# Performance work log

Measured on AMD Instinct MI355X. Metric: run time of the kernel, lower is better.

## Reference

```python
import jax, jax.numpy as jnp
import numpy as np


def setup_inputs() -> dict:
    key = jax.random.key(0)
    k1, k2, k3, k4 = jax.random.split(key, 4)
    H = W = D = 192
    I = jax.random.normal(k1, (1, 1, H, W, D), dtype=jnp.float32)
    dx_t = jax.random.normal(k2, (1, H, W, D), dtype=jnp.float32)
    dy_t = jax.random.normal(k3, (1, H, W, D), dtype=jnp.float32)
    dz_t = jax.random.normal(k4, (1, H, W, D), dtype=jnp.float32)
    return {"I": I, "dx_t": dx_t, "dy_t": dy_t, "dz_t": dz_t}


def reference(I, dx_t, dy_t, dz_t):
    # Trilinear warp, faithful to the torch module (valid for batch=1).
    B, C, H, W, D = I.shape
    # Identity meshgrid: x varies along width (axis 1), y along height (axis 0),
    # z along depth (axis 2) -- matches the numpy construction in __init__.
    x_mesh = jnp.arange(W, dtype=jnp.float32)[None, :, None]
    y_mesh = jnp.arange(H, dtype=jnp.float32)[:, None, None]
    z_mesh = jnp.arange(D, dtype=jnp.float32)[None, None, :]
    # +1 accounts for the zero-padding of I by 1 voxel on every side.
    x = dx_t[0] + x_mesh + 1.0  # [H,W,D]
    y = dy_t[0] + y_mesh + 1.0
    z = dz_t[0] + z_mesh + 1.0

    Ip = jnp.pad(I[0], ((0, 0), (1, 1), (1, 1), (1, 1)))  # [C,H+2,W+2,D+2]
    Hp, Wp, Dp = H + 2, W + 2, D + 2

    fx = jnp.floor(x).astype(jnp.int32)
    fy = jnp.floor(y).astype(jnp.int32)
    fz = jnp.floor(z).astype(jnp.int32)
    x0 = jnp.clip(fx, 0, Wp - 1); x1 = jnp.clip(fx + 1, 0, Wp - 1)
    y0 = jnp.clip(fy, 0, Hp - 1); y1 = jnp.clip(fy + 1, 0, Hp - 1)
    z0 = jnp.clip(fz, 0, Dp - 1); z1 = jnp.clip(fz + 1, 0, Dp - 1)

    # Fractional weights computed from the *clamped* upper corner (faithful).
    dx = x1.astype(jnp.float32) - x
    dy = y1.astype(jnp.float32) - y
    dz = z1.astype(jnp.float32) - z

    # Gather 8 corners: padded volume layout is [C, y, x, z].
    Ia = Ip[:, y0, x0, z0]
    Ib = Ip[:, y1, x0, z0]
    Ic = Ip[:, y0, x1, z0]
    Id = Ip[:, y1, x1, z0]
    Ie = Ip[:, y0, x0, z1]
    If = Ip[:, y1, x0, z1]
    Ig = Ip[:, y0, x1, z1]
    Ih = Ip[:, y1, x1, z1]

    wa = dz * dx * dy
    wb = dz * dx * (1 - dy)
    wc = dz * (1 - dx) * dy
    wd = dz * (1 - dx) * (1 - dy)
    we = (1 - dz) * dx * dy
    wf = (1 - dz) * dx * (1 - dy)
    wg = (1 - dz) * (1 - dx) * dy
    wh = (1 - dz) * (1 - dx) * (1 - dy)

    out = (wa * Ia + wb * Ib + wc * Ic + wd * Id
           + we * Ie + wf * If + wg * Ig + wh * Ih)  # [C,H,W,D]
    return out[None]  # [1,C,H,W,D]
```

## Files before the change

### kernel.cpp

```cpp
#include <hip/hip_runtime.h>

constexpr int H = 192, W = 192, D = 192;
constexpr int BH = 16, BW = 16, BZ = 16;
constexpr int TY = 24, TX = 24, TZ = 28;
constexpr int TILE_N = TY * TX * TZ;
constexpr int NINSTR = TY * TX * (TZ / 4) / 64;

__device__ __forceinline__ float ref_voxel(const float* __restrict__ I,
                                           float x, float y, float zf)
{
    int fx = (int)floorf(x), fy = (int)floorf(y), fz = (int)floorf(zf);
    int x0 = min(max(fx, 0), W + 1), x1 = min(max(fx + 1, 0), W + 1);
    int y0 = min(max(fy, 0), H + 1), y1 = min(max(fy + 1, 0), H + 1);
    int zp0 = min(max(fz, 0), D + 1), zp1 = min(max(fz + 1, 0), D + 1);
    float dx = (float)x1 - x, dy = (float)y1 - y, dz = (float)zp1 - zf;
    int xi0 = x0 - 1, xi1 = x1 - 1, yi0 = y0 - 1, yi1 = y1 - 1;
    int zi = zp0 - 1, zj = zp1 - 1;
    float ax0 = ((unsigned)xi0 < (unsigned)W) ? dx       : 0.f;
    float ax1 = ((unsigned)xi1 < (unsigned)W) ? 1.f - dx : 0.f;
    float ay0 = ((unsigned)yi0 < (unsigned)H) ? dy       : 0.f;
    float ay1 = ((unsigned)yi1 < (unsigned)H) ? 1.f - dy : 0.f;
    float az0 = ((unsigned)zi  < (unsigned)D) ? dz       : 0.f;
    float az1 = ((unsigned)zj  < (unsigned)D) ? 1.f - dz : 0.f;
    int xc0 = min(max(xi0, 0), W - 1), xc1 = min(max(xi1, 0), W - 1);
    int yc0 = min(max(yi0, 0), H - 1), yc1 = min(max(yi1, 0), H - 1);
    int zc0 = min(max(zi, 0), D - 1),  zc1 = min(max(zj, 0), D - 1);
    const float* r00 = I + (yc0 * W + xc0) * D;
    const float* r01 = I + (yc0 * W + xc1) * D;
    const float* r10 = I + (yc1 * W + xc0) * D;
    const float* r11 = I + (yc1 * W + xc1) * D;
    float s00 = az0 * r00[zc0] + az1 * r00[zc1];
    float s01 = az0 * r01[zc0] + az1 * r01[zc1];
    float s10 = az0 * r10[zc0] + az1 * r10[zc1];
    float s11 = az0 * r11[zc0] + az1 * r11[zc1];
    return ay0 * (ax0 * s00 + ax1 * s01) + ay1 * (ax0 * s10 + ax1 * s11);
}

__global__ __launch_bounds__(512) void st_tile(
    const float* __restrict__ I,
    const float* __restrict__ dxt,
    const float* __restrict__ dyt,
    const float* __restrict__ dzt,
    float* __restrict__ out)
{
    __shared__ float tile[TILE_N];

    const int tid = threadIdx.x;
    const int bx = blockIdx.x, by = blockIdx.y, bz = blockIdx.z;
    const int w0 = bx * BW, h0 = by * BH, z0 = bz * BZ;
    const int xg0 = w0 - 4, yg0 = h0 - 4, zg0 = z0 - 4;

    {
        const unsigned wv = tid >> 6, lane = tid & 63;
        for (unsigned i = wv; i < (unsigned)NINSTR; i += 8) {
            unsigned c = i * 64u + lane;
            unsigned row = c / 7u;
            unsigned s = c - row * 7u;
            unsigned ry = row / 24u;
            unsigned rx = row - ry * 24u;
            int gy = min(max(yg0 + (int)ry, 0), H - 1);
            int gx = min(max(xg0 + (int)rx, 0), W - 1);
            int zs = min(max(zg0 + (int)(s * 4u), 0), D - 4);
            const float* src = I + ((gy * W + gx) * D + zs);
            __builtin_amdgcn_global_load_lds(
                (const __attribute__((address_space(1))) void*)src,
                (__attribute__((address_space(3))) void*)(tile + i * 256u),
                16, 0, 0);
        }
    }

    const int zq = tid & 3, wloc = (tid >> 2) & 15, hl0 = tid >> 6;
    const int wg = w0 + wloc;
    float4 vx[2], vy[2], vz[2];
    #pragma unroll
    for (int k = 0; k < 2; ++k) {
        int hg = h0 + hl0 + 8 * k;
        int t4 = (hg * W + wg) * (D / 4) + (z0 >> 2) + zq;
        vx[k] = reinterpret_cast<const float4*>(dxt)[t4];
        vy[k] = reinterpret_cast<const float4*>(dyt)[t4];
        vz[k] = reinterpret_cast<const float4*>(dzt)[t4];
    }

    asm volatile("s_waitcnt vmcnt(0)" ::: "memory");
    __syncthreads();

    const int lox = max(0, -xg0), hix = min(TX - 2, 190 - xg0);
    const int loy = max(0, -yg0), hiy = min(TY - 2, 190 - yg0);
    const int loz = max(0, -zg0), hiz = min(TZ - 2, 190 - zg0);

    float ro[2][4];
    #pragma unroll
    for (int k = 0; k < 2; ++k) {
        const int hg = h0 + hl0 + 8 * k;
        const int hl = hl0 + 8 * k;
        float rxj[4] = {vx[k].x, vx[k].y, vx[k].z, vx[k].w};
        float ryj[4] = {vy[k].x, vy[k].y, vy[k].z, vy[k].w};
        float rzj[4] = {vz[k].x, vz[k].y, vz[k].z, vz[k].w};

        int   lxa[4], lya[4], lza[4];
        float txa[4], tya[4], tza[4];
        bool  fa[4];
        #pragma unroll
        for (int j = 0; j < 4; ++j) {
            float xl = rxj[j] + (float)(wloc + 4);
            float yl = ryj[j] + (float)(hl + 4);
            float zl = rzj[j] + (float)(zq * 4 + j + 4);
            float fxf = floorf(xl), fyf = floorf(yl), fzf = floorf(zl);
            lxa[j] = (int)fxf; lya[j] = (int)fyf; lza[j] = (int)fzf;
            txa[j] = xl - fxf; tya[j] = yl - fyf; tza[j] = zl - fzf;
            fa[j] = ((unsigned)(lxa[j] - lox) <= (unsigned)(hix - lox))
                  & ((unsigned)(lya[j] - loy) <= (unsigned)(hiy - loy))
                  & ((unsigned)(lza[j] - loz) <= (unsigned)(hiz - loz));
        }

        if (__builtin_expect(__all(fa[0] & fa[1] & fa[2] & fa[3]), 1)) {
            #pragma unroll
            for (int j = 0; j < 4; ++j) {
                int b = (lya[j] * TX + lxa[j]) * TZ + lza[j];
                float a0 = tile[b],                a1 = tile[b + 1];
                float b0 = tile[b + TZ],           b1 = tile[b + TZ + 1];
                float c0 = tile[b + TX * TZ],      c1 = tile[b + TX * TZ + 1];
                float d0 = tile[b + TX * TZ + TZ], d1 = tile[b + TX * TZ + TZ + 1];
                float wz0 = 1.f - tza[j], wz1 = tza[j];
                float wx0 = 1.f - txa[j], wx1 = txa[j];
                float wy0 = 1.f - tya[j], wy1 = tya[j];
                float s00 = wz0 * a0 + wz1 * a1;
                float s01 = wz0 * b0 + wz1 * b1;
                float s10 = wz0 * c0 + wz1 * c1;
                float s11 = wz0 * d0 + wz1 * d1;
                ro[k][j] = wy0 * (wx0 * s00 + wx1 * s01) + wy1 * (wx0 * s10 + wx1 * s11);
            }
        } else {
            #pragma unroll
            for (int j = 0; j < 4; ++j) {
                const int zv = z0 + zq * 4 + j;
                float x  = rxj[j] + (float)(wg + 1);
                float y  = ryj[j] + (float)(hg + 1);
                float zf = rzj[j] + (float)(zv + 1);

                int fx = (int)floorf(x), fy = (int)floorf(y), fz = (int)floorf(zf);
                int x0 = min(max(fx, 0), W + 1), x1 = min(max(fx + 1, 0), W + 1);
                int y0 = min(max(fy, 0), H + 1), y1 = min(max(fy + 1, 0), H + 1);
                int zp0 = min(max(fz, 0), D + 1), zp1 = min(max(fz + 1, 0), D + 1);

                float dx = (float)x1 - x, dy = (float)y1 - y, dz = (float)zp1 - zf;

                int xi0 = x0 - 1, xi1 = x1 - 1, yi0 = y0 - 1, yi1 = y1 - 1;
                int zi = zp0 - 1, zj2 = zp1 - 1;

                float ax0 = ((unsigned)xi0 < (unsigned)W) ? dx       : 0.f;
                float ax1 = ((unsigned)xi1 < (unsigned)W) ? 1.f - dx : 0.f;
                float ay0 = ((unsigned)yi0 < (unsigned)H) ? dy       : 0.f;
                float ay1 = ((unsigned)yi1 < (unsigned)H) ? 1.f - dy : 0.f;
                float az0 = ((unsigned)zi  < (unsigned)D) ? dz       : 0.f;
                float az1 = ((unsigned)zj2 < (unsigned)D) ? 1.f - dz : 0.f;

                int xc0 = min(max(xi0, 0), W - 1), xc1 = min(max(xi1, 0), W - 1);
                int yc0 = min(max(yi0, 0), H - 1), yc1 = min(max(yi1, 0), H - 1);
                int zc  = min(max(zi, 0), D - 2);

                bool zlo = (zi <= D - 2);
                bool zhi = (zi >= 0);

                int lx0 = xc0 - xg0, lx1 = xc1 - xg0;
                int ly0 = yc0 - yg0, ly1 = yc1 - yg0;
                int lz  = zc - zg0;

                bool ok = ((unsigned)lx0 <= (unsigned)(TX - 1))
                        & ((unsigned)lx1 <= (unsigned)(TX - 1))
                        & ((unsigned)ly0 <= (unsigned)(TY - 1))
                        & ((unsigned)ly1 <= (unsigned)(TY - 1))
                        & ((unsigned)lz  <= (unsigned)(TZ - 2));

                int b00 = min(max((ly0 * TX + lx0) * TZ + lz, 0), TILE_N - 2);
                int b01 = min(max((ly0 * TX + lx1) * TZ + lz, 0), TILE_N - 2);
                int b10 = min(max((ly1 * TX + lx0) * TZ + lz, 0), TILE_N - 2);
                int b11 = min(max((ly1 * TX + lx1) * TZ + lz, 0), TILE_N - 2);

                float a0 = tile[b00], a1 = tile[b00 + 1];
                float b0 = tile[b01], b1 = tile[b01 + 1];
                float c0 = tile[b10], c1 = tile[b10 + 1];
                float d0 = tile[b11], d1 = tile[b11 + 1];

                float v000 = zlo ? a0 : a1, v001 = zhi ? a1 : a0;
                float v010 = zlo ? b0 : b1, v011 = zhi ? b1 : b0;
                float v100 = zlo ? c0 : c1, v101 = zhi ? c1 : c0;
                float v110 = zlo ? d0 : d1, v111 = zhi ? d1 : d0;
                float s00 = az0 * v000 + az1 * v001;
                float s01 = az0 * v010 + az1 * v011;
                float s10 = az0 * v100 + az1 * v101;
                float s11 = az0 * v110 + az1 * v111;
                float r = ay0 * (ax0 * s00 + ax1 * s01)
                        + ay1 * (ax0 * s10 + ax1 * s11);

                ro[k][j] = __builtin_expect(ok, 1) ? r : ref_voxel(I, x, y, zf);
            }
        }
    }

    #pragma unroll
    for (int k = 0; k < 2; ++k) {
        int hg = h0 + hl0 + 8 * k;
        int t4 = (hg * W + wg) * (D / 4) + (z0 >> 2) + zq;
        reinterpret_cast<float4*>(out)[t4] =
            make_float4(ro[k][0], ro[k][1], ro[k][2], ro[k][3]);
    }
}

extern "C" void kernel_launch(void* const* d_in, const int* in_sizes, int n_in,
                              void* d_out, int out_size, void* d_ws, size_t ws_size,
                              hipStream_t stream) {
    const float* I   = (const float*)d_in[0];
    const float* dxt = (const float*)d_in[1];
    const float* dyt = (const float*)d_in[2];
    const float* dzt = (const float*)d_in[3];
    float* out = (float*)d_out;

    dim3 grid(W / BW, H / BH, D / BZ);
    hipLaunchKernelGGL(st_tile, grid, dim3(512), 0, stream,
                       I, dxt, dyt, dzt, out);
}
```

Measured before the change: 50.00 us.

## Shrink LDS halo tile and split staging to overlap second half with compute

Shrinks the staged halo tile from 24x24x28 to 23x23x24, with an asymmetric x/y halo, to cut LDS usage and global loads per block. Staging is split into two phases: the first 40 load instructions plus the first half's displacement loads are waited on with a partial vmcnt, and the first half computes while the remaining tile rows arrive. Launch bounds now request 6 blocks per CU for more occupancy. The smaller halo pushes more voxels onto the slow fallback path, and the hand-counted vmcnt values are fragile.

Result: slower. 102.5 us (+104.9%).

```diff
diff --git a/kernel.cpp b/kernel.cpp
--- a/kernel.cpp
+++ b/kernel.cpp
@@ -2,9 +2,11 @@
 
 constexpr int H = 192, W = 192, D = 192;
 constexpr int BH = 16, BW = 16, BZ = 16;
-constexpr int TY = 24, TX = 24, TZ = 28;
-constexpr int TILE_N = TY * TX * TZ;
-constexpr int NINSTR = TY * TX * (TZ / 4) / 64;
+constexpr int TY = 23, TX = 23, TZ = 24;
+constexpr int TILE_DATA = TY * TX * TZ;
+constexpr int LDS_DWORDS = 3264 * 4;
+constexpr int BMAX = TILE_DATA - 2;
+constexpr int NB1 = 40;
 
 __device__ __forceinline__ float ref_voxel(const float* __restrict__ I,
                                            float x, float y, float zf)
@@ -36,74 +38,91 @@
     return ay0 * (ax0 * s00 + ax1 * s01) + ay1 * (ax0 * s10 + ax1 * s11);
 }
 
-__global__ __launch_bounds__(512) void st_tile(
+__device__ __forceinline__ void stage_instr(const float* __restrict__ I, float* tile,
+                                            unsigned i, unsigned lane,
+                                            int xg0, int yg0, int zg0)
+{
+    unsigned c = i * 64u + lane;
+    unsigned row = c / 6u;
+    unsigned s = c - row * 6u;
+    unsigned ry = row / 23u;
+    unsigned rx = row - ry * 23u;
+    int gy = min(max(yg0 + (int)min(ry, 22u), 0), H - 1);
+    int gx = min(max(xg0 + (int)rx, 0), W - 1);
+    int zs = min(max(zg0 + (int)(s * 4u), 0), D - 4);
+    const float* src = I + ((gy * W + gx) * D + zs);
+    __builtin_amdgcn_global_load_lds(
+        (const __attribute__((address_space(1))) void*)src,
+        (__attribute__((address_space(3))) void*)(tile + i * 256u),
+        16, 0, 0);
+}
+
+__global__ __launch_bounds__(512, 6) void st_tile(
     const float* __restrict__ I,
     const float* __restrict__ dxt,
     const float* __restrict__ dyt,
     const float* __restrict__ dzt,
     float* __restrict__ out)
 {
-    __shared__ float tile[TILE_N];
+    __shared__ float tile[LDS_DWORDS];
 
     const int tid = threadIdx.x;
     const int bx = blockIdx.x, by = blockIdx.y, bz = blockIdx.z;
     const int w0 = bx * BW, h0 = by * BH, z0 = bz * BZ;
-    const int xg0 = w0 - 4, yg0 = h0 - 4, zg0 = z0 - 4;
-
-    {
-        const unsigned wv = tid >> 6, lane = tid & 63;
-        for (unsigned i = wv; i < (unsigned)NINSTR; i += 8) {
-            unsigned c = i * 64u + lane;
-            unsigned row = c / 7u;
-            unsigned s = c - row * 7u;
-            unsigned ry = row / 24u;
-            unsigned rx = row - ry * 24u;
-            int gy = min(max(yg0 + (int)ry, 0), H - 1);
-            int gx = min(max(xg0 + (int)rx, 0), W - 1);
-            int zs = min(max(zg0 + (int)(s * 4u), 0), D - 4);
-            const float* src = I + ((gy * W + gx) * D + zs);
-            __builtin_amdgcn_global_load_lds(
-                (const __attribute__((address_space(1))) void*)src,
-                (__attribute__((address_space(3))) void*)(tile + i * 256u),
-                16, 0, 0);
-        }
-    }
-
+    const int xg0 = w0 - 3, yg0 = h0 - 3, zg0 = z0 - 4;
+
+    const unsigned wv = tid >> 6, lane = tid & 63;
     const int zq = tid & 3, wloc = (tid >> 2) & 15, hl0 = tid >> 6;
     const int wg = w0 + wloc;
-    float4 vx[2], vy[2], vz[2];
+
     #pragma unroll
-    for (int k = 0; k < 2; ++k) {
-        int hg = h0 + hl0 + 8 * k;
-        int t4 = (hg * W + wg) * (D / 4) + (z0 >> 2) + zq;
-        vx[k] = reinterpret_cast<const float4*>(dxt)[t4];
-        vy[k] = reinterpret_cast<const float4*>(dyt)[t4];
-        vz[k] = reinterpret_cast<const float4*>(dzt)[t4];
-    }
-
-    asm volatile("s_waitcnt vmcnt(0)" ::: "memory");
-    __syncthreads();
+    for (unsigned t = 0; t < 5; ++t)
+        stage_instr(I, tile, wv + 8u * t, lane, xg0, yg0, zg0);
+    __builtin_amdgcn_sched_barrier(0);
+
+    const int t40 = ((h0 + hl0) * W + wg) * (D / 4) + (z0 >> 2) + zq;
+    float4 vx0 = reinterpret_cast<const float4*>(dxt)[t40];
+    float4 vy0 = reinterpret_cast<const float4*>(dyt)[t40];
+    float4 vz0 = reinterpret_cast<const float4*>(dzt)[t40];
+    __builtin_amdgcn_sched_barrier(0);
+
+    stage_instr(I, tile, 40u + wv, lane, xg0, yg0, zg0);
+    if (wv < 3) stage_instr(I, tile, 48u + wv, lane, xg0, yg0, zg0);
+    __builtin_amdgcn_sched_barrier(0);
+
+    const int t41 = ((h0 + 8 + hl0) * W + wg) * (D / 4) + (z0 >> 2) + zq;
+    float4 vx1 = reinterpret_cast<const float4*>(dxt)[t41];
+    float4 vy1 = reinterpret_cast<const float4*>(dyt)[t41];
+    float4 vz1 = reinterpret_cast<const float4*>(dzt)[t41];
+    __builtin_amdgcn_sched_barrier(0);
+
+    asm volatile("s_waitcnt vmcnt(4)" ::: "memory");
+    __builtin_amdgcn_s_barrier();
+    __builtin_amdgcn_sched_barrier(0);
 
     const int lox = max(0, -xg0), hix = min(TX - 2, 190 - xg0);
     const int loy = max(0, -yg0), hiy = min(TY - 2, 190 - yg0);
     const int loz = max(0, -zg0), hiz = min(TZ - 2, 190 - zg0);
 
-    float ro[2][4];
     #pragma unroll
-    for (int k = 0; k < 2; ++k) {
-        const int hg = h0 + hl0 + 8 * k;
-        const int hl = hl0 + 8 * k;
-        float rxj[4] = {vx[k].x, vx[k].y, vx[k].z, vx[k].w};
-        float ryj[4] = {vy[k].x, vy[k].y, vy[k].z, vy[k].w};
-        float rzj[4] = {vz[k].x, vz[k].y, vz[k].z, vz[k].w};
+    for (int half = 0; half < 2; ++half) {
+        const int hl = hl0 + half * 8;
+        const int hg = h0 + hl;
+        float4 vx = half ? vx1 : vx0;
+        float4 vy = half ? vy1 : vy0;
+        float4 vz = half ? vz1 : vz0;
+        float rxj[4] = {vx.x, vx.y, vx.z, vx.w};
+        float ryj[4] = {vy.x, vy.y, vy.z, vy.w};
+        float rzj[4] = {vz.x, vz.y, vz.z, vz.w};
+        float ro[4];
 
         int   lxa[4], lya[4], lza[4];
         float txa[4], tya[4], tza[4];
         bool  fa[4];
         #pragma unroll
         for (int j = 0; j < 4; ++j) {
-            float xl = rxj[j] + (float)(wloc + 4);
-            float yl = ryj[j] + (float)(hl + 4);
+            float xl = rxj[j] + (float)(wloc + 3);
+            float yl = ryj[j] + (float)(hl + 3);
             float zl = rzj[j] + (float)(zq * 4 + j + 4);
             float fxf = floorf(xl), fyf = floorf(yl), fzf = floorf(zl);
             lxa[j] = (int)fxf; lya[j] = (int)fyf; lza[j] = (int)fzf;
@@ -128,7 +147,7 @@
                 float s01 = wz0 * b0 + wz1 * b1;
                 float s10 = wz0 * c0 + wz1 * c1;
                 float s11 = wz0 * d0 + wz1 * d1;
-                ro[k][j] = wy0 * (wx0 * s00 + wx1 * s01) + wy1 * (wx0 * s10 + wx1 * s11);
+                ro[j] = wy0 * (wx0 * s00 + wx1 * s01) + wy1 * (wx0 * s10 + wx1 * s11);
             }
         } else {
             #pragma unroll
@@ -172,10 +191,10 @@
                         & ((unsigned)ly1 <= (unsigned)(TY - 1))
                         & ((unsigned)lz  <= (unsigned)(TZ - 2));
 
-                int b00 = min(max((ly0 * TX + lx0) * TZ + lz, 0), TILE_N - 2);
-                int b01 = min(max((ly0 * TX + lx1) * TZ + lz, 0), TILE_N - 2);
-                int b10 = min(max((ly1 * TX + lx0) * TZ + lz, 0), TILE_N - 2);
-                int b11 = min(max((ly1 * TX + lx1) * TZ + lz, 0), TILE_N - 2);
+                int b00 = min(max((ly0 * TX + lx0) * TZ + lz, 0), BMAX);
+                int b01 = min(max((ly0 * TX + lx1) * TZ + lz, 0), BMAX);
+                int b10 = min(max((ly1 * TX + lx0) * TZ + lz, 0), BMAX);
+                int b11 = min(max((ly1 * TX + lx1) * TZ + lz, 0), BMAX);
 
                 float a0 = tile[b00], a1 = tile[b00 + 1];
                 float b0 = tile[b01], b1 = tile[b01 + 1];
@@ -193,17 +212,18 @@
                 float r = ay0 * (ax0 * s00 + ax1 * s01)
                         + ay1 * (ax0 * s10 + ax1 * s11);
 
-                ro[k][j] = __builtin_expect(ok, 1) ? r : ref_voxel(I, x, y, zf);
+                ro[j] = __builtin_expect(ok, 1) ? r : ref_voxel(I, x, y, zf);
             }
         }
-    }
-
-    #pragma unroll
-    for (int k = 0; k < 2; ++k) {
-        int hg = h0 + hl0 + 8 * k;
-        int t4 = (hg * W + wg) * (D / 4) + (z0 >> 2) + zq;
-        reinterpret_cast<float4*>(out)[t4] =
-            make_float4(ro[k][0], ro[k][1], ro[k][2], ro[k][3]);
+
+        reinterpret_cast<float4*>(out)[half ? t41 : t40] =
+            make_float4(ro[0], ro[1], ro[2], ro[3]);
+
+        if (half == 0) {
+            asm volatile("s_waitcnt vmcnt(1)" ::: "memory");
+            __builtin_amdgcn_s_barrier();
+            __builtin_amdgcn_sched_barrier(0);
+        }
     }
 }
 
```
